# Kernel optimization log

Hardware: AMD Instinct MI355X
Metric: run time of the kernel (lower is better)

The kernel has to match this reference:

```python
import jax, jax.numpy as jnp
import numpy as np
import math

HEAD_DIM = 128
N_HEADS = 32
HIDDEN = 4096
ROPE_THETA = 10000.0
NEG = -100000.0


def _rope_cos_sin(pos):
    # pos: [B, L] int -> cos, sin: [B, L, HEAD_DIM]
    inv_freq = 1.0 / (ROPE_THETA ** (jnp.arange(0, HEAD_DIM, 2, dtype=jnp.float32) / HEAD_DIM))
    freqs = pos.astype(jnp.float32)[..., None] * inv_freq  # [B, L, HEAD_DIM//2]
    emb = jnp.concatenate([freqs, freqs], axis=-1)
    return jnp.cos(emb), jnp.sin(emb)


def _rotate_half(x):
    x1, x2 = x[..., : HEAD_DIM // 2], x[..., HEAD_DIM // 2 :]
    return jnp.concatenate([-x2, x1], axis=-1)


def _apply_rope(h, cos, sin):
    # h: [B, H, L, D], cos/sin: [B, L, D] -> unsqueeze head dim
    return h * cos[:, None] + _rotate_half(h) * sin[:, None]


def setup_inputs() -> dict:
    key = jax.random.key(0)
    ks = jax.random.split(key, 8)
    B, Q, K = 2, 1024, 2048
    inp = {
        "hidden_states": jax.random.normal(ks[0], (B, Q, HIDDEN), jnp.float32),
        "key_value_states": jax.random.normal(ks[1], (B, K, HIDDEN), jnp.float32),
        "Wq": jax.random.normal(ks[2], (HIDDEN, HIDDEN), jnp.float32) * 0.02,
        "Wk": jax.random.normal(ks[3], (HIDDEN, HIDDEN), jnp.float32) * 0.02,
        "Wv": jax.random.normal(ks[4], (HIDDEN, HIDDEN), jnp.float32) * 0.02,
        "Wo": jax.random.normal(ks[5], (HIDDEN, HIDDEN), jnp.float32) * 0.02,
        "position_ids": jnp.arange(B * Q, dtype=jnp.int32).reshape(B, Q),
        "text_position_ids": jnp.arange(B * K, dtype=jnp.int32).reshape(B, K),
        "simul_mask_idx": jnp.sort(jax.random.randint(ks[6], (B, Q), 0, K, jnp.int32), axis=-1),
        "window_size": jax.random.randint(ks[7], (B, Q), 0, 512, jnp.int32),
    }
    return inp


def reference(hidden_states, key_value_states, Wq, Wk, Wv, Wo,
              position_ids, text_position_ids, simul_mask_idx, window_size):
    B, Qlen, _ = hidden_states.shape
    Klen = key_value_states.shape[1]

    q = jnp.einsum('bqh,hd->bqd', hidden_states, Wq.T).reshape(B, Qlen, N_HEADS, HEAD_DIM).transpose(0, 2, 1, 3)
    k = jnp.einsum('bkh,hd->bkd', key_value_states, Wk.T).reshape(B, Klen, N_HEADS, HEAD_DIM).transpose(0, 2, 1, 3)
    v = jnp.einsum('bkh,hd->bkd', key_value_states, Wv.T).reshape(B, Klen, N_HEADS, HEAD_DIM).transpose(0, 2, 1, 3)

    cos, sin = _rope_cos_sin(position_ids)
    q = _apply_rope(q, cos, sin)
    t_cos, t_sin = _rope_cos_sin(text_position_ids)
    k = _apply_rope(k, t_cos, t_sin)

    scores = jnp.einsum('bhqd,bhkd->bhqk', q, k) / math.sqrt(HEAD_DIM)

    # simul windowed mask: key j visible for query i iff clamp(idx-w,0) <= j < idx
    idx = simul_mask_idx[:, None, :, None]          # [B,1,Q,1]
    w = window_size[:, None, :, None]               # [B,1,Q,1]
    tmp = jnp.arange(Klen, dtype=jnp.int32)         # [K]
    mask = (jnp.clip(idx - w, 0) <= tmp) & (tmp < idx)  # [B,1,Q,K]
    scores = jnp.where(mask, scores, NEG)

    probs = jax.nn.softmax(scores.astype(jnp.float32), axis=-1).astype(q.dtype)
    attn = jnp.einsum('bhqk,bhkd->bhqd', probs, v)
    attn = attn.transpose(0, 2, 1, 3).reshape(B, Qlen, HIDDEN)
    out = jnp.einsum('bqh,hd->bqd', attn, Wo.T)
    return out
```

## Files before the change

### kernel.cpp

```cpp
#include <hip/hip_runtime.h>
#include <stdint.h>

#define BATCH 2
#define QLEN 1024
#define KLEN 2048
#define NH 32
#define HD 128
#define HID 4096

typedef short bf16x8 __attribute__((ext_vector_type(8)));
typedef float f32x4 __attribute__((ext_vector_type(4)));
typedef unsigned short u16;

typedef const __attribute__((address_space(1))) void gvoid;
typedef __attribute__((address_space(3))) void lvoid;

__device__ __forceinline__ u16 f2bf(float f) {
  union { float f; uint32_t u; } x; x.f = f;
  uint32_t r = x.u + 0x7fffu + ((x.u >> 16) & 1u);
  return (u16)(r >> 16);
}
__device__ __forceinline__ float bf2f(u16 h) {
  union { uint32_t u; float f; } x; x.u = ((uint32_t)h) << 16;
  return x.f;
}
__device__ __forceinline__ f32x4 mfma16(bf16x8 a, bf16x8 b, f32x4 c) {
  return __builtin_amdgcn_mfma_f32_16x16x32_bf16(a, b, c, 0, 0, 0);
}
__device__ __forceinline__ void glds16(const u16* src, char* dst) {
  __builtin_amdgcn_global_load_lds((gvoid*)src, (lvoid*)dst, 16, 0, 0);
}

__global__ __launch_bounds__(256) void cvt_kernel(const float* __restrict__ in,
                                                  u16* __restrict__ out, int n) {
  int i = (blockIdx.x * 256 + threadIdx.x) * 8;
  if (i >= n) return;
  const float4* p = (const float4*)(in + i);
  float4 a = p[0], b = p[1];
  union { u16 h[8]; bf16x8 v; } u;
  u.h[0] = f2bf(a.x); u.h[1] = f2bf(a.y); u.h[2] = f2bf(a.z); u.h[3] = f2bf(a.w);
  u.h[4] = f2bf(b.x); u.h[5] = f2bf(b.y); u.h[6] = f2bf(b.z); u.h[7] = f2bf(b.w);
  *(bf16x8*)(out + i) = u.v;
}

#define RD_A(CB, ks, mf) (*(const bf16x8*)(lds + (CB) + (ks) * 16384 + (mf) * 1024 + rA))
#define RD_B(CB, ks, nf) (*(const bf16x8*)(lds + 65536 + (CB) + (ks) * 16384 + (nf) * 1024 + rB))

#define TILE256(CB, NB, K0N)                                                     \
  {                                                                              \
    bf16x8 af[4], bfr[4], af2[4];                                                \
    _Pragma("unroll") for (int x = 0; x < 4; x++) af[x] = RD_A(CB, 0, x);        \
    _Pragma("unroll") for (int x = 0; x < 4; x++) bfr[x] = RD_B(CB, 0, x);       \
    glds16(As0 + (K0N), dA + (NB));                                              \
    glds16(As1 + (K0N), dA + (NB) + 8192);                                       \
    glds16(Bs0 + (K0N), dB + (NB));                                              \
    glds16(Bs1 + (K0N), dB + (NB) + 8192);                                       \
    __builtin_amdgcn_s_barrier();                                                \
    asm volatile("s_waitcnt lgkmcnt(0)" ::: "memory");                           \
    __builtin_amdgcn_sched_barrier(0);                                           \
    __builtin_amdgcn_s_setprio(1);                                               \
    _Pragma("unroll") for (int mf = 0; mf < 4; mf++)                             \
      _Pragma("unroll") for (int nf = 0; nf < 4; nf++)                           \
        acc[mf][nf] = mfma16(af[mf], bfr[nf], acc[mf][nf]);                      \
    __builtin_amdgcn_s_setprio(0);                                               \
    __builtin_amdgcn_s_barrier();                                                \
    _Pragma("unroll") for (int x = 0; x < 4; x++) af2[x] = RD_A(CB, 0, 4 + x);   \
    glds16(As0 + (K0N) + 32, dA + (NB) + 16384);                                 \
    glds16(As1 + (K0N) + 32, dA + (NB) + 16384 + 8192);                          \
    asm volatile("s_waitcnt vmcnt(6)" ::: "memory");                             \
    __builtin_amdgcn_s_barrier();                                                \
    asm volatile("s_waitcnt lgkmcnt(0)" ::: "memory");                           \
    __builtin_amdgcn_sched_barrier(0);                                           \
    __builtin_amdgcn_s_setprio(1);                                               \
    _Pragma("unroll") for (int mf = 0; mf < 4; mf++)                             \
      _Pragma("unroll") for (int nf = 0; nf < 4; nf++)                           \
        acc[4 + mf][nf] = mfma16(af2[mf], bfr[nf], acc[4 + mf][nf]);             \
    __builtin_amdgcn_s_setprio(0);                                               \
    __builtin_amdgcn_s_barrier();                                                \
    _Pragma("unroll") for (int x = 0; x < 4; x++) af[x] = RD_A(CB, 1, x);        \
    _Pragma("unroll") for (int x = 0; x < 4; x++) bfr[x] = RD_B(CB, 1, x);       \
    glds16(Bs0 + (K0N) + 32, dB + (NB) + 16384);                                 \
    glds16(Bs1 + (K0N) + 32, dB + (NB) + 16384 + 8192);                          \
    __builtin_amdgcn_s_barrier();                                                \
    asm volatile("s_waitcnt lgkmcnt(0)" ::: "memory");                           \
    __builtin_amdgcn_sched_barrier(0);                                           \
    __builtin_amdgcn_s_setprio(1);                                               \
    _Pragma("unroll") for (int mf = 0; mf < 4; mf++)                             \
      _Pragma("unroll") for (int nf = 0; nf < 4; nf++)                           \
        acc[mf][nf] = mfma16(af[mf], bfr[nf], acc[mf][nf]);                      \
    __builtin_amdgcn_s_setprio(0);                                               \
    __builtin_amdgcn_s_barrier();                                                \
    _Pragma("unroll") for (int x = 0; x < 4; x++) af2[x] = RD_A(CB, 1, 4 + x);   \
    asm volatile("s_waitcnt vmcnt(4)" ::: "memory");                             \
    __builtin_amdgcn_s_barrier();                                                \
    asm volatile("s_waitcnt lgkmcnt(0)" ::: "memory");                           \
    __builtin_amdgcn_sched_barrier(0);                                           \
    __builtin_amdgcn_s_setprio(1);                                               \
    _Pragma("unroll") for (int mf = 0; mf < 4; mf++)                             \
      _Pragma("unroll") for (int nf = 0; nf < 4; nf++)                           \
        acc[4 + mf][nf] = mfma16(af2[mf], bfr[nf], acc[4 + mf][nf]);             \
    __builtin_amdgcn_s_setprio(0);                                               \
    __builtin_amdgcn_s_barrier();                                                \
  }

template <int EPI>
__global__ __launch_bounds__(512, 2) void gemm256(const u16* __restrict__ A,
                                                  const u16* __restrict__ Bw,
                                                  void* __restrict__ Cout,
                                                  int M, int N, int K) {
  (void)M;
  __shared__ alignas(16) char lds[131072];
  const int tid = threadIdx.x;
  const int lane = tid & 63, wv = tid >> 6;
  const int wvm = wv >> 2, wvn = wv & 3;
  const int g = lane >> 4, l16 = lane & 15;
  const int m0 = blockIdx.y * 256, n0 = blockIdx.x * 256;

  const int srow = tid >> 2;
  const int sg = (tid & 3) ^ ((srow >> 1) & 3);
  const u16* As0 = A + (size_t)(m0 + srow) * K + sg * 8;
  const u16* As1 = A + (size_t)(m0 + 128 + srow) * K + sg * 8;
  const u16* Bs0 = Bw + (size_t)(n0 + srow) * K + sg * 8;
  const u16* Bs1 = Bw + (size_t)(n0 + 128 + srow) * K + sg * 8;
  char* dA = lds + tid * 16;
  char* dB = lds + 65536 + tid * 16;

  const int rsw = (g ^ ((l16 >> 1) & 3)) << 4;
  const int rA = (wvm * 128 + l16) * 64 + rsw;
  const int rB = (wvn * 64 + l16) * 64 + rsw;

  f32x4 acc[8][4];
#pragma unroll
  for (int mf = 0; mf < 8; mf++)
#pragma unroll
    for (int nf = 0; nf < 4; nf++) acc[mf][nf] = (f32x4){0.f, 0.f, 0.f, 0.f};

  glds16(As0, dA);
  glds16(As1, dA + 8192);
  glds16(Bs0, dB);
  glds16(Bs1, dB + 8192);
  glds16(As0 + 32, dA + 16384);
  glds16(As1 + 32, dA + 16384 + 8192);
  glds16(Bs0 + 32, dB + 16384);
  glds16(Bs1 + 32, dB + 16384 + 8192);
  asm volatile("s_waitcnt vmcnt(4)" ::: "memory");
  __builtin_amdgcn_s_barrier();

  const int NT = K >> 6;
  for (int t = 0; t < NT; t += 2) {
    const int kA = (t + 1) * 64;
    TILE256(0, 32768, kA)
    const int kB = (((t + 2) < NT) ? (t + 2) : 0) * 64;
    TILE256(32768, 0, kB)
  }

  if (EPI == 2) {
    u16* C = (u16*)Cout;
#pragma unroll
    for (int mf = 0; mf < 8; mf++) {
      int rowb = m0 + wvm * 128 + mf * 16 + g * 4;
#pragma unroll
      for (int nf = 0; nf < 4; nf++) {
        int col = n0 + wvn * 64 + nf * 16 + l16;
#pragma unroll
        for (int j = 0; j < 4; j++)
          C[(size_t)(rowb + j) * N + col] = f2bf(acc[mf][nf][j]);
      }
    }
  } else {
    u16* C = (u16*)Cout;
#pragma unroll
    for (int mf = 0; mf < 8; mf++) {
      int rowb = m0 + wvm * 128 + mf * 16 + g * 4;
      int bb = rowb >> 11, tt = rowb & 2047;
#pragma unroll
      for (int nf = 0; nf < 4; nf++) {
        int col = n0 + wvn * 64 + nf * 16 + l16;
        uint64_t pk = (uint64_t)f2bf(acc[mf][nf][0]) |
                      ((uint64_t)f2bf(acc[mf][nf][1]) << 16) |
                      ((uint64_t)f2bf(acc[mf][nf][2]) << 32) |
                      ((uint64_t)f2bf(acc[mf][nf][3]) << 48);
        *(uint64_t*)(C + ((size_t)(bb * 4096 + col)) * 2048 + tt) = pk;
      }
    }
  }
}

#define RD_AT(BUF, ks, mf) \
  (*(const bf16x8*)(lds + (BUF) * 32768 + (ks) * 16384 + (mf) * 1024 + rA))
#define RD_BT(BUF, ks, nf) \
  (*(const bf16x8*)(lds + 98304 + (BUF) * 16384 + (ks) * 8192 + (nf) * 1024 + rB))

#define STG_H0(BUF, K0N)                                    \
  glds16(AsT0 + (K0N), dAT + (BUF) * 32768);                \
  glds16(AsT1 + (K0N), dAT + (BUF) * 32768 + 8192);         \
  glds16(BsT0 + (K0N), dBT + (BUF) * 16384);

#define STG_H1(BUF, K0N)                                    \
  glds16(AsT0 + (K0N) + 32, dAT + (BUF) * 32768 + 16384);   \
  glds16(AsT1 + (K0N) + 32, dAT + (BUF) * 32768 + 16384 + 8192); \
  glds16(BsT0 + (K0N) + 32, dBT + (BUF) * 16384 + 8192);

#define TILE256T(CUR, STG, K0N)                                                  \
  {                                                                              \
    bf16x8 af[4], bfr[4];                                                        \
    _Pragma("unroll") for (int x = 0; x < 4; x++) af[x] = RD_AT(CUR, 0, x);      \
    _Pragma("unroll") for (int x = 0; x < 4; x++) bfr[x] = RD_BT(CUR, 0, x);     \
    STG_H0(STG, K0N)                                                             \
    __builtin_amdgcn_s_barrier();                                                \
    asm volatile("s_waitcnt lgkmcnt(0)" ::: "memory");                           \
    __builtin_amdgcn_sched_barrier(0);                                           \
    __builtin_amdgcn_s_setprio(1);                                               \
    _Pragma("unroll") for (int mf = 0; mf < 4; mf++)                             \
      _Pragma("unroll") for (int nf = 0; nf < 4; nf++)                           \
        acc[mf][nf] = mfma16(af[mf], bfr[nf], acc[mf][nf]);                      \
    __builtin_amdgcn_s_setprio(0);                                               \
    __builtin_amdgcn_s_barrier();                                                \
    _Pragma("unroll") for (int x = 0; x < 4; x++) af[x] = RD_AT(CUR, 1, x);      \
    _Pragma("unroll") for (int x = 0; x < 4; x++) bfr[x] = RD_BT(CUR, 1, x);     \
    STG_H1(STG, K0N)                                                             \
    asm volatile("s_waitcnt vmcnt(6)" ::: "memory");                             \
    __builtin_amdgcn_s_barrier();                                                \
    asm volatile("s_waitcnt lgkmcnt(0)" ::: "memory");                           \
    __builtin_amdgcn_sched_barrier(0);                                           \
    __builtin_amdgcn_s_setprio(1);                                               \
    _Pragma("unroll") for (int mf = 0; mf < 4; mf++)                             \
      _Pragma("unroll") for (int nf = 0; nf < 4; nf++)                           \
        acc[mf][nf] = mfma16(af[mf], bfr[nf], acc[mf][nf]);                      \
    __builtin_amdgcn_s_setprio(0);                                               \
    __builtin_amdgcn_s_barrier();                                                \
  }

template <int EPI>
__global__ __launch_bounds__(512, 2) void gemm256T(const u16* __restrict__ W,
                                                   const u16* __restrict__ Act,
                                                   void* __restrict__ Cout) {
  const int K = HID;
  __shared__ alignas(16) char lds[147456];
  const int tid = threadIdx.x;
  const int lane = tid & 63, wv = tid >> 6;
  const int wvm = wv >> 1, wvn = wv & 1;
  const int g = lane >> 4, l16 = lane & 15;
  const int m0 = blockIdx.y * 256;
  const int n0 = blockIdx.x * 128;

  const int srow = tid >> 2;
  const int sg = (tid & 3) ^ ((srow >> 1) & 3);
  const u16* AsT0 = W + (size_t)(m0 + srow) * K + sg * 8;
  const u16* AsT1 = W + (size_t)(m0 + 128 + srow) * K + sg * 8;
  const u16* BsT0 = Act + (size_t)(n0 + srow) * K + sg * 8;
  char* dAT = lds + tid * 16;
  char* dBT = lds + 98304 + tid * 16;

  const int rsw = (g ^ ((l16 >> 1) & 3)) << 4;
  const int rA = (wvm * 64 + l16) * 64 + rsw;
  const int rB = (wvn * 64 + l16) * 64 + rsw;

  f32x4 acc[4][4];
#pragma unroll
  for (int mf = 0; mf < 4; mf++)
#pragma unroll
    for (int nf = 0; nf < 4; nf++) acc[mf][nf] = (f32x4){0.f, 0.f, 0.f, 0.f};

  STG_H0(0, 0)
  STG_H1(0, 0)
  STG_H0(1, 64)
  STG_H1(1, 64)
  asm volatile("s_waitcnt vmcnt(6)" ::: "memory");
  __builtin_amdgcn_s_barrier();

  for (int t = 0; t < 63; t += 3) {
    const int k1 = (t + 2) * 64;
    const int k2 = (t + 3) * 64;
    const int k3 = ((t + 4) < 64) ? (t + 4) * 64 : 0;
    TILE256T(0, 2, k1)
    TILE256T(1, 0, k2)
    TILE256T(2, 1, k3)
  }
  {
    bf16x8 af[4], bfr[4];
#pragma unroll
    for (int x = 0; x < 4; x++) af[x] = RD_AT(0, 0, x);
#pragma unroll
    for (int x = 0; x < 4; x++) bfr[x] = RD_BT(0, 0, x);
#pragma unroll
    for (int mf = 0; mf < 4; mf++)
#pragma unroll
      for (int nf = 0; nf < 4; nf++)
        acc[mf][nf] = mfma16(af[mf], bfr[nf], acc[mf][nf]);
#pragma unroll
    for (int x = 0; x < 4; x++) af[x] = RD_AT(0, 1, x);
#pragma unroll
    for (int x = 0; x < 4; x++) bfr[x] = RD_BT(0, 1, x);
#pragma unroll
    for (int mf = 0; mf < 4; mf++)
#pragma unroll
      for (int nf = 0; nf < 4; nf++)
        acc[mf][nf] = mfma16(af[mf], bfr[nf], acc[mf][nf]);
  }

  if (EPI == 0) {
    float* C = (float*)Cout;
#pragma unroll
    for (int mf = 0; mf < 4; mf++) {
      int frow = m0 + wvm * 64 + mf * 16 + g * 4;
#pragma unroll
      for (int nf = 0; nf < 4; nf++) {
        int col = n0 + wvn * 64 + nf * 16 + l16;
        float4 v = {acc[mf][nf][0], acc[mf][nf][1], acc[mf][nf][2], acc[mf][nf][3]};
        *(float4*)(C + (size_t)col * HID + frow) = v;
      }
    }
  } else {
    u16* C = (u16*)Cout;
#pragma unroll
    for (int mf = 0; mf < 4; mf++) {
      int frow = m0 + wvm * 64 + mf * 16 + g * 4;
#pragma unroll
      for (int nf = 0; nf < 4; nf++) {
        int col = n0 + wvn * 64 + nf * 16 + l16;
        uint64_t pk = (uint64_t)f2bf(acc[mf][nf][0]) |
                      ((uint64_t)f2bf(acc[mf][nf][1]) << 16) |
                      ((uint64_t)f2bf(acc[mf][nf][2]) << 32) |
                      ((uint64_t)f2bf(acc[mf][nf][3]) << 48);
        *(uint64_t*)(C + (size_t)col * HID + frow) = pk;
      }
    }
  }
}

__global__ __launch_bounds__(256) void rope_kernel(const u16* __restrict__ x,
                                                   const int* __restrict__ pos,
                                                   u16* __restrict__ out,
                                                   int rowsPerB) {
  int row = blockIdx.x;
  int b = row / rowsPerB, r = row - b * rowsPerB;
  float p = (float)pos[row];
  int t = threadIdx.x;
  int h = t >> 3, i0 = (t & 7) * 8;
  const u16* xr = x + (size_t)row * HID + h * HD;
  bf16x8 lov = *(const bf16x8*)(xr + i0);
  bf16x8 hiv = *(const bf16x8*)(xr + 64 + i0);
  union { u16 h[8]; bf16x8 v; } olo, ohi;
#pragma unroll
  for (int j = 0; j < 8; j++) {
    float lo = bf2f((u16)lov[j]);
    float hi = bf2f((u16)hiv[j]);
    float f = exp2f(-(float)(i0 + j) * (13.287712379549449f / 64.0f));
    float ang = p * f;
    float s, c;
    sincosf(ang, &s, &c);
    olo.h[j] = f2bf(lo * c - hi * s);
    ohi.h[j] = f2bf(hi * c + lo * s);
  }
  u16* ob = out + ((size_t)((b * NH + h) * rowsPerB) + r) * HD;
  *(bf16x8*)(ob + i0) = olo.v;
  *(bf16x8*)(ob + 64 + i0) = ohi.v;
}

__global__ __launch_bounds__(256) void vmean_kernel(const u16* __restrict__ vt,
                                                    float* __restrict__ vm) {
  int row = blockIdx.x * 4 + (threadIdx.x >> 6);
  int lane = threadIdx.x & 63;
  const u16* p = vt + (size_t)row * KLEN;
  float s = 0.f;
#pragma unroll
  for (int it = 0; it < 4; it++) {
    bf16x8 v = *(const bf16x8*)(p + it * 512 + lane * 8);
#pragma unroll
    for (int j = 0; j < 8; j++) s += bf2f((u16)v[j]);
  }
  for (int off = 32; off; off >>= 1) s += __shfl_xor(s, off);
  if (lane == 0) vm[row] = s * (1.0f / (float)KLEN);
}

__global__ __launch_bounds__(256, 2) void attn_kernel(
    const u16* __restrict__ qb, const u16* __restrict__ kb,
    const u16* __restrict__ vt, const float* __restrict__ vm,
    const int* __restrict__ idxA, const int* __restrict__ wA,
    u16* __restrict__ aout) {
  __shared__ u16 Ks[32][136];
  __shared__ u16 Vs[128][40];
  __shared__ u16 Ps[4][16][40];
  __shared__ int sS[64], sE[64], sRange[2];

  const int tid = threadIdx.x, lane = tid & 63, wv = tid >> 6;
  const int g = lane >> 4, l16 = lane & 15;
  const int blk = blockIdx.x;
  const int qt = blk & 15, bh = blk >> 4, b = bh >> 5, h = bh & 31;
  const int q0 = qt * 64;
  const float SCALE = 0.08838834764831845f;

  if (tid < 64) {
    int e = idxA[b * QLEN + q0 + tid];
    int w = wA[b * QLEN + q0 + tid];
    int s = e - w;
    if (s < 0) s = 0;
    sS[tid] = s;
    sE[tid] = e;
  }
  __syncthreads();
  if (wv == 0) {
    int s_ = sS[lane], e_ = sE[lane];
    int mn = (e_ > s_) ? s_ : 0x7fffffff;
    int mx = (e_ > s_) ? e_ : 0;
    for (int off = 32; off; off >>= 1) {
      mn = min(mn, __shfl_xor(mn, off));
      mx = max(mx, __shfl_xor(mx, off));
    }
    if (lane == 0) { sRange[0] = mn; sRange[1] = mx; }
  }
  __syncthreads();
  const int klo = sRange[0], khi = sRange[1];

  int rs[4], re[4];
#pragma unroll
  for (int r = 0; r < 4; r++) {
    rs[r] = sS[wv * 16 + g * 4 + r];
    re[r] = sE[wv * 16 + g * 4 + r];
  }

  bf16x8 qf[4];
  {
    const u16* qp = qb + ((size_t)(bh * QLEN + q0 + wv * 16 + l16)) * HD + g * 8;
#pragma unroll
    for (int s4 = 0; s4 < 4; s4++) qf[s4] = *(const bf16x8*)(qp + s4 * 32);
  }

  f32x4 acc[8];
#pragma unroll
  for (int db = 0; db < 8; db++) acc[db] = (f32x4){0.f, 0.f, 0.f, 0.f};
  float mrow[4] = {-1e30f, -1e30f, -1e30f, -1e30f};
  float lsum[4] = {0.f, 0.f, 0.f, 0.f};

  if (klo < khi) {
    for (int t0 = (klo & ~31); t0 < khi; t0 += 32) {
      {
        int idx = tid * 8;
        int kr = idx >> 7, kc = idx & 127;
        *(bf16x8*)(&Ks[kr][kc]) =
            *(const bf16x8*)(kb + ((size_t)(bh * KLEN + t0 + kr)) * HD + kc);
        int kr2 = kr + 16;
        *(bf16x8*)(&Ks[kr2][kc]) =
            *(const bf16x8*)(kb + ((size_t)(bh * KLEN + t0 + kr2)) * HD + kc);
        int vr = idx >> 5, vc = idx & 31;
        *(bf16x8*)(&Vs[vr][vc]) =
            *(const bf16x8*)(vt + ((size_t)(bh * HD + vr)) * KLEN + t0 + vc);
        int vr2 = vr + 64;
        *(bf16x8*)(&Vs[vr2][vc]) =
            *(const bf16x8*)(vt + ((size_t)(bh * HD + vr2)) * KLEN + t0 + vc);
      }
      __syncthreads();

      f32x4 sc0 = (f32x4){0.f, 0.f, 0.f, 0.f};
      f32x4 sc1 = (f32x4){0.f, 0.f, 0.f, 0.f};
#pragma unroll
      for (int s4 = 0; s4 < 4; s4++) {
        bf16x8 k0 = *(const bf16x8*)(&Ks[l16][s4 * 32 + g * 8]);
        bf16x8 k1 = *(const bf16x8*)(&Ks[16 + l16][s4 * 32 + g * 8]);
        sc0 = mfma16(qf[s4], k0, sc0);
        sc1 = mfma16(qf[s4], k1, sc1);
      }

      float resc[4];
#pragma unroll
      for (int r = 0; r < 4; r++) {
        float v0 = sc0[r] * SCALE, v1 = sc1[r] * SCALE;
        int t_0 = t0 + l16, t_1 = t0 + 16 + l16;
        v0 = (t_0 >= rs[r] && t_0 < re[r]) ? v0 : -1e30f;
        v1 = (t_1 >= rs[r] && t_1 < re[r]) ? v1 : -1e30f;
        float mx = fmaxf(v0, v1);
        mx = fmaxf(mx, __shfl_xor(mx, 1));
        mx = fmaxf(mx, __shfl_xor(mx, 2));
        mx = fmaxf(mx, __shfl_xor(mx, 4));
        mx = fmaxf(mx, __shfl_xor(mx, 8));
        float mn = fmaxf(mrow[r], mx);
        float rc = __expf(mrow[r] - mn);
        float p0 = __expf(v0 - mn), p1 = __expf(v1 - mn);
        mrow[r] = mn;
        resc[r] = rc;
        float ps = p0 + p1;
        ps += __shfl_xor(ps, 1);
        ps += __shfl_xor(ps, 2);
        ps += __shfl_xor(ps, 4);
        ps += __shfl_xor(ps, 8);
        lsum[r] = lsum[r] * rc + ps;
        Ps[wv][g * 4 + r][l16] = f2bf(p0);
        Ps[wv][g * 4 + r][16 + l16] = f2bf(p1);
      }
#pragma unroll
      for (int db = 0; db < 8; db++) {
#pragma unroll
        for (int r = 0; r < 4; r++) acc[db][r] *= resc[r];
      }
      bf16x8 pf = *(const bf16x8*)(&Ps[wv][l16][g * 8]);
#pragma unroll
      for (int db = 0; db < 8; db++) {
        bf16x8 vf = *(const bf16x8*)(&Vs[db * 16 + l16][g * 8]);
        acc[db] = mfma16(pf, vf, acc[db]);
      }
      __syncthreads();
    }
  }

#pragma unroll
  for (int r = 0; r < 4; r++) {
    int lr = wv * 16 + g * 4 + r;
    int q = q0 + lr;
    bool empty = (re[r] <= rs[r]);
    float inv = empty ? 0.f : 1.0f / lsum[r];
    u16* orow = aout + ((size_t)(b * QLEN + q)) * HID + h * HD;
#pragma unroll
    for (int db = 0; db < 8; db++) {
      float o = empty ? vm[bh * HD + db * 16 + l16] : acc[db][r] * inv;
      orow[db * 16 + l16] = f2bf(o);
    }
  }
}

extern "C" void kernel_launch(void* const* d_in, const int* in_sizes, int n_in,
                              void* d_out, int out_size, void* d_ws, size_t ws_size,
                              hipStream_t stream) {
  (void)in_sizes; (void)n_in; (void)out_size; (void)ws_size;
  const float* hs = (const float*)d_in[0];
  const float* kvs = (const float*)d_in[1];
  const float* Wq = (const float*)d_in[2];
  const float* Wk = (const float*)d_in[3];
  const float* Wv = (const float*)d_in[4];
  const float* Wo = (const float*)d_in[5];
  const int* pos = (const int*)d_in[6];
  const int* tpos = (const int*)d_in[7];
  const int* sidx = (const int*)d_in[8];
  const int* wsz = (const int*)d_in[9];
  float* out = (float*)d_out;

  char* ws = (char*)d_ws;
  size_t off = 0;
  auto alloc = [&](size_t bytes) -> void* {
    void* p = ws + off;
    off += (bytes + 255) & ~(size_t)255;
    return p;
  };
  const size_t WN = (size_t)HID * HID;
  const size_t NQ = (size_t)BATCH * QLEN * HID;
  const size_t NK = (size_t)BATCH * KLEN * HID;

  u16* wbuf = (u16*)alloc(WN * 2);
  u16* hid_b = (u16*)alloc(NQ * 2);
  u16* kv_b = (u16*)alloc(NK * 2);
  u16* sc_b = (u16*)alloc(NK * 2);
  u16* q_b = (u16*)alloc(NQ * 2);
  u16* k_b = (u16*)alloc(NK * 2);
  u16* vt_b = (u16*)alloc(NK * 2);
  float* vmean = (float*)alloc((size_t)BATCH * NH * HD * 4);

  cvt_kernel<<<(int)(NQ / 2048), 256, 0, stream>>>(hs, hid_b, (int)NQ);
  cvt_kernel<<<(int)(NK / 2048), 256, 0, stream>>>(kvs, kv_b, (int)NK);

  cvt_kernel<<<(int)(WN / 2048), 256, 0, stream>>>(Wq, wbuf, (int)WN);
  gemm256T<2><<<dim3(BATCH * QLEN / 128, HID / 256), 512, 0, stream>>>(
      wbuf, hid_b, sc_b);
  rope_kernel<<<BATCH * QLEN, 256, 0, stream>>>(sc_b, pos, q_b, QLEN);

  cvt_kernel<<<(int)(WN / 2048), 256, 0, stream>>>(Wk, wbuf, (int)WN);
  gemm256<2><<<dim3(HID / 256, BATCH * KLEN / 256), 512, 0, stream>>>(
      kv_b, wbuf, sc_b, BATCH * KLEN, HID, HID);
  rope_kernel<<<BATCH * KLEN, 256, 0, stream>>>(sc_b, tpos, k_b, KLEN);

  cvt_kernel<<<(int)(WN / 2048), 256, 0, stream>>>(Wv, wbuf, (int)WN);
  gemm256<1><<<dim3(HID / 256, BATCH * KLEN / 256), 512, 0, stream>>>(
      kv_b, wbuf, vt_b, BATCH * KLEN, HID, HID);
  vmean_kernel<<<BATCH * NH * HD / 4, 256, 0, stream>>>(vt_b, vmean);

  attn_kernel<<<BATCH * NH * (QLEN / 64), 256, 0, stream>>>(
      q_b, k_b, vt_b, vmean, sidx, wsz, sc_b);

  cvt_kernel<<<(int)(WN / 2048), 256, 0, stream>>>(Wo, wbuf, (int)WN);
  gemm256T<0><<<dim3(BATCH * QLEN / 128, HID / 256), 512, 0, stream>>>(
      wbuf, sc_b, out);
}
```

Measured before the change: 586.1 us.

## Fuse K/V projections into one GEMM, batch conversions, swizzle tiles, merge rope/vmean

```diff
diff --git a/kernel.cpp b/kernel.cpp
--- a/kernel.cpp
+++ b/kernel.cpp
@@ -31,16 +31,33 @@
   __builtin_amdgcn_global_load_lds((gvoid*)src, (lvoid*)dst, 16, 0, 0);
 }
 
-__global__ __launch_bounds__(256) void cvt_kernel(const float* __restrict__ in,
-                                                  u16* __restrict__ out, int n) {
-  int i = (blockIdx.x * 256 + threadIdx.x) * 8;
-  if (i >= n) return;
+__device__ __forceinline__ void cvt8(const float* in, u16* out, int i) {
   const float4* p = (const float4*)(in + i);
   float4 a = p[0], b = p[1];
   union { u16 h[8]; bf16x8 v; } u;
   u.h[0] = f2bf(a.x); u.h[1] = f2bf(a.y); u.h[2] = f2bf(a.z); u.h[3] = f2bf(a.w);
   u.h[4] = f2bf(b.x); u.h[5] = f2bf(b.y); u.h[6] = f2bf(b.z); u.h[7] = f2bf(b.w);
   *(bf16x8*)(out + i) = u.v;
+}
+
+__global__ __launch_bounds__(256) void cvt_kernel(const float* __restrict__ in,
+                                                  u16* __restrict__ out, int n) {
+  int i = (blockIdx.x * 256 + threadIdx.x) * 8;
+  if (i >= n) return;
+  cvt8(in, out, i);
+}
+
+__global__ __launch_bounds__(256) void cvt2_kernel(const float* __restrict__ s0,
+                                                   u16* __restrict__ d0, int n0,
+                                                   const float* __restrict__ s1,
+                                                   u16* __restrict__ d1, int n1) {
+  int i = (blockIdx.x * 256 + threadIdx.x) * 8;
+  if (i < n0) {
+    cvt8(s0, d0, i);
+  } else {
+    int j = i - n0;
+    if (j < n1) cvt8(s1, d1, j);
+  }
 }
 
 #define RD_A(CB, ks, mf) (*(const bf16x8*)(lds + (CB) + (ks) * 16384 + (mf) * 1024 + rA))
@@ -53,8 +70,6 @@
     _Pragma("unroll") for (int x = 0; x < 4; x++) bfr[x] = RD_B(CB, 0, x);       \
     glds16(As0 + (K0N), dA + (NB));                                              \
     glds16(As1 + (K0N), dA + (NB) + 8192);                                       \
-    glds16(Bs0 + (K0N), dB + (NB));                                              \
-    glds16(Bs1 + (K0N), dB + (NB) + 8192);                                       \
     __builtin_amdgcn_s_barrier();                                                \
     asm volatile("s_waitcnt lgkmcnt(0)" ::: "memory");                           \
     __builtin_amdgcn_sched_barrier(0);                                           \
@@ -65,9 +80,9 @@
     __builtin_amdgcn_s_setprio(0);                                               \
     __builtin_amdgcn_s_barrier();                                                \
     _Pragma("unroll") for (int x = 0; x < 4; x++) af2[x] = RD_A(CB, 0, 4 + x);   \
-    glds16(As0 + (K0N) + 32, dA + (NB) + 16384);                                 \
-    glds16(As1 + (K0N) + 32, dA + (NB) + 16384 + 8192);                          \
-    asm volatile("s_waitcnt vmcnt(6)" ::: "memory");                             \
+    glds16(Bs0 + (K0N), dB + (NB));                                              \
+    glds16(Bs1 + (K0N), dB + (NB) + 8192);                                       \
+    asm volatile("s_waitcnt vmcnt(4)" ::: "memory");                             \
     __builtin_amdgcn_s_barrier();                                                \
     asm volatile("s_waitcnt lgkmcnt(0)" ::: "memory");                           \
     __builtin_amdgcn_sched_barrier(0);                                           \
@@ -79,8 +94,8 @@
     __builtin_amdgcn_s_barrier();                                                \
     _Pragma("unroll") for (int x = 0; x < 4; x++) af[x] = RD_A(CB, 1, x);        \
     _Pragma("unroll") for (int x = 0; x < 4; x++) bfr[x] = RD_B(CB, 1, x);       \
-    glds16(Bs0 + (K0N) + 32, dB + (NB) + 16384);                                 \
-    glds16(Bs1 + (K0N) + 32, dB + (NB) + 16384 + 8192);                          \
+    glds16(As0 + (K0N) + 32, dA + (NB) + 16384);                                 \
+    glds16(As1 + (K0N) + 32, dA + (NB) + 16384 + 8192);                          \
     __builtin_amdgcn_s_barrier();                                                \
     asm volatile("s_waitcnt lgkmcnt(0)" ::: "memory");                           \
     __builtin_amdgcn_sched_barrier(0);                                           \
@@ -91,6 +106,8 @@
     __builtin_amdgcn_s_setprio(0);                                               \
     __builtin_amdgcn_s_barrier();                                                \
     _Pragma("unroll") for (int x = 0; x < 4; x++) af2[x] = RD_A(CB, 1, 4 + x);   \
+    glds16(Bs0 + (K0N) + 32, dB + (NB) + 16384);                                 \
+    glds16(Bs1 + (K0N) + 32, dB + (NB) + 16384 + 8192);                          \
     asm volatile("s_waitcnt vmcnt(4)" ::: "memory");                             \
     __builtin_amdgcn_s_barrier();                                                \
     asm volatile("s_waitcnt lgkmcnt(0)" ::: "memory");                           \
@@ -103,25 +120,28 @@
     __builtin_amdgcn_s_barrier();                                                \
   }
 
-template <int EPI>
-__global__ __launch_bounds__(512, 2) void gemm256(const u16* __restrict__ A,
-                                                  const u16* __restrict__ Bw,
-                                                  void* __restrict__ Cout,
-                                                  int M, int N, int K) {
-  (void)M;
+__global__ __launch_bounds__(512, 2) void gemm256kv(const u16* __restrict__ A,
+                                                    const u16* __restrict__ Bw,
+                                                    u16* __restrict__ Ck,
+                                                    u16* __restrict__ Cvt) {
+  const int K = HID;
   __shared__ alignas(16) char lds[131072];
   const int tid = threadIdx.x;
   const int lane = tid & 63, wv = tid >> 6;
   const int wvm = wv >> 2, wvn = wv & 3;
   const int g = lane >> 4, l16 = lane & 15;
-  const int m0 = blockIdx.y * 256, n0 = blockIdx.x * 256;
+
+  const int lin = blockIdx.y * 32 + blockIdx.x;
+  const int swz = (lin & 7) * 64 + (lin >> 3);
+  const int m0 = (swz >> 5) * 256;
+  const int n0g = (swz & 31) * 256;
 
   const int srow = tid >> 2;
   const int sg = (tid & 3) ^ ((srow >> 1) & 3);
   const u16* As0 = A + (size_t)(m0 + srow) * K + sg * 8;
   const u16* As1 = A + (size_t)(m0 + 128 + srow) * K + sg * 8;
-  const u16* Bs0 = Bw + (size_t)(n0 + srow) * K + sg * 8;
-  const u16* Bs1 = Bw + (size_t)(n0 + 128 + srow) * K + sg * 8;
+  const u16* Bs0 = Bw + (size_t)(n0g + srow) * K + sg * 8;
+  const u16* Bs1 = Bw + (size_t)(n0g + 128 + srow) * K + sg * 8;
   char* dA = lds + tid * 16;
   char* dB = lds + 65536 + tid * 16;
 
@@ -154,33 +174,31 @@
     TILE256(32768, 0, kB)
   }
 
-  if (EPI == 2) {
-    u16* C = (u16*)Cout;
+  if (n0g < 4096) {
 #pragma unroll
     for (int mf = 0; mf < 8; mf++) {
       int rowb = m0 + wvm * 128 + mf * 16 + g * 4;
 #pragma unroll
       for (int nf = 0; nf < 4; nf++) {
-        int col = n0 + wvn * 64 + nf * 16 + l16;
+        int col = n0g + wvn * 64 + nf * 16 + l16;
 #pragma unroll
         for (int j = 0; j < 4; j++)
-          C[(size_t)(rowb + j) * N + col] = f2bf(acc[mf][nf][j]);
+          Ck[(size_t)(rowb + j) * HID + col] = f2bf(acc[mf][nf][j]);
       }
     }
   } else {
-    u16* C = (u16*)Cout;
 #pragma unroll
     for (int mf = 0; mf < 8; mf++) {
       int rowb = m0 + wvm * 128 + mf * 16 + g * 4;
       int bb = rowb >> 11, tt = rowb & 2047;
 #pragma unroll
       for (int nf = 0; nf < 4; nf++) {
-        int col = n0 + wvn * 64 + nf * 16 + l16;
+        int colv = (n0g - 4096) + wvn * 64 + nf * 16 + l16;
         uint64_t pk = (uint64_t)f2bf(acc[mf][nf][0]) |
                       ((uint64_t)f2bf(acc[mf][nf][1]) << 16) |
                       ((uint64_t)f2bf(acc[mf][nf][2]) << 32) |
                       ((uint64_t)f2bf(acc[mf][nf][3]) << 48);
-        *(uint64_t*)(C + ((size_t)(bb * 4096 + col)) * 2048 + tt) = pk;
+        *(uint64_t*)(Cvt + ((size_t)(bb * 4096 + colv)) * 2048 + tt) = pk;
       }
     }
   }
@@ -241,8 +259,11 @@
   const int lane = tid & 63, wv = tid >> 6;
   const int wvm = wv >> 1, wvn = wv & 1;
   const int g = lane >> 4, l16 = lane & 15;
-  const int m0 = blockIdx.y * 256;
-  const int n0 = blockIdx.x * 128;
+
+  const int lin = blockIdx.y * 16 + blockIdx.x;
+  const int swz = (lin & 7) * 32 + (lin >> 3);
+  const int m0 = (swz >> 4) * 256;
+  const int n0 = (swz & 15) * 128;
 
   const int srow = tid >> 2;
   const int sg = (tid & 3) ^ ((srow >> 1) & 3);
@@ -329,14 +350,9 @@
   }
 }
 
-__global__ __launch_bounds__(256) void rope_kernel(const u16* __restrict__ x,
-                                                   const int* __restrict__ pos,
-                                                   u16* __restrict__ out,
-                                                   int rowsPerB) {
-  int row = blockIdx.x;
+__device__ __forceinline__ void rope_row(const u16* x, float p, u16* out,
+                                         int rowsPerB, int row, int t) {
   int b = row / rowsPerB, r = row - b * rowsPerB;
-  float p = (float)pos[row];
-  int t = threadIdx.x;
   int h = t >> 3, i0 = (t & 7) * 8;
   const u16* xr = x + (size_t)row * HID + h * HD;
   bf16x8 lov = *(const bf16x8*)(xr + i0);
@@ -358,20 +374,33 @@
   *(bf16x8*)(ob + 64 + i0) = ohi.v;
 }
 
-__global__ __launch_bounds__(256) void vmean_kernel(const u16* __restrict__ vt,
-                                                    float* __restrict__ vm) {
-  int row = blockIdx.x * 4 + (threadIdx.x >> 6);
-  int lane = threadIdx.x & 63;
-  const u16* p = vt + (size_t)row * KLEN;
-  float s = 0.f;
-#pragma unroll
-  for (int it = 0; it < 4; it++) {
-    bf16x8 v = *(const bf16x8*)(p + it * 512 + lane * 8);
-#pragma unroll
-    for (int j = 0; j < 8; j++) s += bf2f((u16)v[j]);
-  }
-  for (int off = 32; off; off >>= 1) s += __shfl_xor(s, off);
-  if (lane == 0) vm[row] = s * (1.0f / (float)KLEN);
+__global__ __launch_bounds__(256) void rope_vmean_kernel(
+    const u16* __restrict__ qsrc, const u16* __restrict__ ksrc,
+    u16* __restrict__ qdst, u16* __restrict__ kdst,
+    const int* __restrict__ pos, const int* __restrict__ tpos,
+    const u16* __restrict__ vt, float* __restrict__ vm) {
+  int bid = blockIdx.x;
+  if (bid >= 6144) {
+    int row = (bid - 6144) * 4 + (threadIdx.x >> 6);
+    int lane = threadIdx.x & 63;
+    const u16* p = vt + (size_t)row * KLEN;
+    float s = 0.f;
+#pragma unroll
+    for (int it = 0; it < 4; it++) {
+      bf16x8 v = *(const bf16x8*)(p + it * 512 + lane * 8);
+#pragma unroll
+      for (int j = 0; j < 8; j++) s += bf2f((u16)v[j]);
+    }
+    for (int off = 32; off; off >>= 1) s += __shfl_xor(s, off);
+    if (lane == 0) vm[row] = s * (1.0f / (float)KLEN);
+    return;
+  }
+  if (bid < 2048) {
+    rope_row(qsrc, (float)pos[bid], qdst, QLEN, bid, threadIdx.x);
+  } else {
+    int row = bid - 2048;
+    rope_row(ksrc, (float)tpos[row], kdst, KLEN, row, threadIdx.x);
+  }
 }
 
 __global__ __launch_bounds__(256, 2) void attn_kernel(
@@ -545,37 +574,31 @@
   const size_t NQ = (size_t)BATCH * QLEN * HID;
   const size_t NK = (size_t)BATCH * KLEN * HID;
 
-  u16* wbuf = (u16*)alloc(WN * 2);
+  u16* wbig = (u16*)alloc(2 * WN * 2);
   u16* hid_b = (u16*)alloc(NQ * 2);
   u16* kv_b = (u16*)alloc(NK * 2);
   u16* sc_b = (u16*)alloc(NK * 2);
+  u16* qp_b = (u16*)alloc(NQ * 2);
   u16* q_b = (u16*)alloc(NQ * 2);
   u16* k_b = (u16*)alloc(NK * 2);
   u16* vt_b = (u16*)alloc(NK * 2);
   float* vmean = (float*)alloc((size_t)BATCH * NH * HD * 4);
 
-  cvt_kernel<<<(int)(NQ / 2048), 256, 0, stream>>>(hs, hid_b, (int)NQ);
-  cvt_kernel<<<(int)(NK / 2048), 256, 0, stream>>>(kvs, kv_b, (int)NK);
-
-  cvt_kernel<<<(int)(WN / 2048), 256, 0, stream>>>(Wq, wbuf, (int)WN);
-  gemm256T<2><<<dim3(BATCH * QLEN / 128, HID / 256), 512, 0, stream>>>(
-      wbuf, hid_b, sc_b);
-  rope_kernel<<<BATCH * QLEN, 256, 0, stream>>>(sc_b, pos, q_b, QLEN);
-
-  cvt_kernel<<<(int)(WN / 2048), 256, 0, stream>>>(Wk, wbuf, (int)WN);
-  gemm256<2><<<dim3(HID / 256, BATCH * KLEN / 256), 512, 0, stream>>>(
-      kv_b, wbuf, sc_b, BATCH * KLEN, HID, HID);
-  rope_kernel<<<BATCH * KLEN, 256, 0, stream>>>(sc_b, tpos, k_b, KLEN);
-
-  cvt_kernel<<<(int)(WN / 2048), 256, 0, stream>>>(Wv, wbuf, (int)WN);
-  gemm256<1><<<dim3(HID / 256, BATCH * KLEN / 256), 512, 0, stream>>>(
-      kv_b, wbuf, vt_b, BATCH * KLEN, HID, HID);
-  vmean_kernel<<<BATCH * NH * HD / 4, 256, 0, stream>>>(vt_b, vmean);
+  cvt2_kernel<<<(int)((NQ + NK) / 2048), 256, 0, stream>>>(hs, hid_b, (int)NQ,
+                                                           kvs, kv_b, (int)NK);
+  cvt_kernel<<<(int)(WN / 2048), 256, 0, stream>>>(Wq, wbig, (int)WN);
+  gemm256T<2><<<dim3(16, 16), 512, 0, stream>>>(wbig, hid_b, qp_b);
+
+  cvt2_kernel<<<(int)(2 * WN / 2048), 256, 0, stream>>>(Wk, wbig, (int)WN,
+                                                        Wv, wbig + WN, (int)WN);
+  gemm256kv<<<dim3(32, 16), 512, 0, stream>>>(kv_b, wbig, sc_b, vt_b);
+
+  rope_vmean_kernel<<<8192, 256, 0, stream>>>(qp_b, sc_b, q_b, k_b, pos, tpos,
+                                              vt_b, vmean);
 
   attn_kernel<<<BATCH * NH * (QLEN / 64), 256, 0, stream>>>(
       q_b, k_b, vt_b, vmean, sidx, wsz, sc_b);
 
-  cvt_kernel<<<(int)(WN / 2048), 256, 0, stream>>>(Wo, wbuf, (int)WN);
-  gemm256T<0><<<dim3(BATCH * QLEN / 128, HID / 256), 512, 0, stream>>>(
-      wbuf, sc_b, out);
-}
+  cvt_kernel<<<(int)(WN / 2048), 256, 0, stream>>>(Wo, wbig, (int)WN);
+  gemm256T<0><<<dim3(16, 16), 512, 0, stream>>>(wbig, sc_b, out);
+}
```

After: 604.1 us. 1.03x slower.
